# Kernel tuning notes

Hardware: AMD Instinct MI355X
Metric: run time of the kernel (lower is better)

## Reference

```python
import jax, jax.numpy as jnp
from jax import lax
import numpy as np

BATCH, T, IN_DIM, RES = 32, 2048, 64, 1024
SPECTRAL_RADIUS, SPARSITY, INPUT_SCALING, LEAK = 1.2, 0.2, 0.5, 0.3


def setup_inputs() -> dict:
    key = jax.random.key(0)
    inputs = jax.random.normal(key, (BATCH, T, IN_DIM), dtype=jnp.float32)
    # Replicate the layer's build(): fixed random reservoir, seeded numpy RNG.
    rng = np.random.RandomState(42)
    W_in = rng.uniform(-INPUT_SCALING, INPUT_SCALING, size=(IN_DIM, RES)).astype(np.float32)
    W_res = rng.randn(RES, RES)
    mask = rng.rand(RES, RES) < SPARSITY
    W_res *= mask
    sr = np.max(np.abs(np.linalg.eigvals(W_res)))
    if sr > 0:
        W_res *= SPECTRAL_RADIUS / sr
    return {
        "inputs": inputs,
        "W_in": jnp.asarray(W_in),
        "W_res": jnp.asarray(W_res.astype(np.float32)),
    }


def reference(inputs, W_in, W_res):
    # inputs: [B, T, I]; W_in: [I, R]; W_res: [R, R]
    leak = jnp.asarray(LEAK, inputs.dtype)
    # Hoist the input projection out of the recurrence (same math, one big GEMM).
    x_proj = jnp.einsum("bti,ir->btr", inputs, W_in)  # [B, T, R]
    state0 = jnp.zeros((inputs.shape[0], W_res.shape[0]), dtype=inputs.dtype)

    def step(state, x_t):  # x_t: [B, R]
        new_state = jnp.tanh(x_t + state @ W_res)
        state = (1.0 - leak) * state + leak * new_state
        return state, state

    _, states = lax.scan(step, state0, jnp.swapaxes(x_proj, 0, 1))  # [T, B, R]
    return jnp.swapaxes(states, 0, 1)  # [B, T, R] (return_sequences=True)
```

## Files before the change

kernel.cpp:

```cpp
#include <hip/hip_runtime.h>

#define T_STEPS 2048
#define NBATCH  32
#define IN_DIM  64
#define RES     1024
#define LEAKF   0.3f
#define NCG     64
#define NBG     4

typedef unsigned int u32;
typedef unsigned long long u64cp;

__global__ __launch_bounds__(256, 1) void esn_persist(
    const float* __restrict__ inp,
    const float* __restrict__ Win,
    const float* __restrict__ Wres,
    float* __restrict__ out,
    float* __restrict__ sC,
    u32* __restrict__ cnts)
{
    const int tid   = threadIdx.x;
    const int c_loc = tid & 15;
    const int ks    = tid >> 4;
    const int cg    = blockIdx.x;
    const int bg    = blockIdx.y;
    const int c0    = cg * 16;
    const int b0    = bg * 8;
    const int c     = c0 + c_loc;

    float w[64];
    {
        const float* wp = Wres + (size_t)(ks * 64) * RES + c;
        #pragma unroll
        for (int j = 0; j < 64; ++j) w[j] = wp[(size_t)j * RES];
    }

    __shared__ __align__(16) float sst[8256];
    __shared__ float pl[16][8][17];

    u32* cnt = cnts + bg * 64;
    float* sCb = sC + (size_t)bg * 2 * RES * 8;

    const int fb = tid >> 4;
    float s_prev = 0.f;

    for (int t = 0; t < T_STEPS; ++t) {
        float* sCr = sCb + ((t & 1) ^ 1) * (RES * 8);
        float* sCw = sCb + (t & 1) * (RES * 8);

        float x = 0.f;
        if (tid < 128) {
            const float* inb = inp + ((size_t)(b0 + fb) * T_STEPS + t) * IN_DIM;
            #pragma unroll
            for (int i = 0; i < IN_DIM; i += 4) {
                const float4 v = *reinterpret_cast<const float4*>(inb + i);
                x = fmaf(v.x, Win[(size_t)(i + 0) * RES + c], x);
                x = fmaf(v.y, Win[(size_t)(i + 1) * RES + c], x);
                x = fmaf(v.z, Win[(size_t)(i + 2) * RES + c], x);
                x = fmaf(v.w, Win[(size_t)(i + 3) * RES + c], x);
            }
        }

        if (t > 0) {
            if (tid == 0) {
                const u32 tgt = 64u * (u32)t;
                while (__hip_atomic_load(cnt, __ATOMIC_RELAXED,
                                         __HIP_MEMORY_SCOPE_AGENT) < tgt) {
                    __builtin_amdgcn_s_sleep(1);
                }
            }
            __syncthreads();

            #pragma unroll
            for (int i = 0; i < 8; ++i) {
                const int m = i * 256 + tid;
                u64cp lo = __hip_atomic_load((u64cp*)(sCr + (size_t)m * 4),
                                             __ATOMIC_RELAXED, __HIP_MEMORY_SCOPE_AGENT);
                u64cp hi = __hip_atomic_load((u64cp*)(sCr + (size_t)m * 4 + 2),
                                             __ATOMIC_RELAXED, __HIP_MEMORY_SCOPE_AGENT);
                float4* dst = (float4*)((char*)sst + (size_t)m * 16 + (m >> 7) * 16);
                *dst = make_float4(__uint_as_float((unsigned)(lo       )),
                                   __uint_as_float((unsigned)(lo >> 32u)),
                                   __uint_as_float((unsigned)(hi       )),
                                   __uint_as_float((unsigned)(hi >> 32u)));
            }
            __syncthreads();
        }

        float acc0 = 0.f, acc1 = 0.f, acc2 = 0.f, acc3 = 0.f;
        float acc4 = 0.f, acc5 = 0.f, acc6 = 0.f, acc7 = 0.f;
        if (t > 0) {
            const char* base = (const char*)sst + (size_t)(ks * 64) * 32 + ks * 16;
            #pragma unroll
            for (int j = 0; j < 64; ++j) {
                const float4 sa = *reinterpret_cast<const float4*>(base + j * 32);
                const float4 sb = *reinterpret_cast<const float4*>(base + j * 32 + 16);
                const float wj = w[j];
                acc0 = fmaf(sa.x, wj, acc0);
                acc1 = fmaf(sa.y, wj, acc1);
                acc2 = fmaf(sa.z, wj, acc2);
                acc3 = fmaf(sa.w, wj, acc3);
                acc4 = fmaf(sb.x, wj, acc4);
                acc5 = fmaf(sb.y, wj, acc5);
                acc6 = fmaf(sb.z, wj, acc6);
                acc7 = fmaf(sb.w, wj, acc7);
            }
        }

        pl[ks][0][c_loc] = acc0;
        pl[ks][1][c_loc] = acc1;
        pl[ks][2][c_loc] = acc2;
        pl[ks][3][c_loc] = acc3;
        pl[ks][4][c_loc] = acc4;
        pl[ks][5][c_loc] = acc5;
        pl[ks][6][c_loc] = acc6;
        pl[ks][7][c_loc] = acc7;
        __syncthreads();

        if (tid < 128) {
            float sum = 0.f;
            #pragma unroll
            for (int q = 0; q < 16; ++q) sum += pl[q][fb][c_loc];

            const float nw = tanhf(x + sum);
            const float sn = fmaf(1.0f - LEAKF, s_prev, LEAKF * nw);
            s_prev = sn;

            out[((size_t)(b0 + fb) * T_STEPS + t) * RES + c] = sn;
            __hip_atomic_store(sCw + (size_t)c * 8 + fb, sn,
                               __ATOMIC_RELAXED, __HIP_MEMORY_SCOPE_AGENT);
        }
        __syncthreads();

        if (tid == 0)
            __hip_atomic_fetch_add(cnt, 1u, __ATOMIC_RELAXED,
                                   __HIP_MEMORY_SCOPE_AGENT);
    }
}

__global__ __launch_bounds__(256) void esn_step(
    const float* __restrict__ inp,
    const float* __restrict__ Win,
    const float* __restrict__ Wres,
    float* __restrict__ out,
    float* __restrict__ sT,
    int t)
{
    const int tid   = threadIdx.x;
    const int c_loc = tid & 15;
    const int ks    = tid >> 4;
    const int c0    = blockIdx.x * 16;
    const int b0    = blockIdx.y * 8;
    const int c     = c0 + c_loc;

    const float* sTr = sT + ((t & 1) ^ 1) * (RES * NBATCH);
    float*       sTw = sT + (t & 1) * (RES * NBATCH);

    float acc0 = 0.f, acc1 = 0.f, acc2 = 0.f, acc3 = 0.f;
    float acc4 = 0.f, acc5 = 0.f, acc6 = 0.f, acc7 = 0.f;

    if (t > 0) {
        const int kbeg = ks * 64;
        const float* wp = Wres + (size_t)kbeg * RES + c;
        const float* sp = sTr + kbeg * NBATCH + b0;
        #pragma unroll 4
        for (int j = 0; j < 64; ++j) {
            const float w = wp[(size_t)j * RES];
            const float4 sa = *reinterpret_cast<const float4*>(sp + j * NBATCH);
            const float4 sb = *reinterpret_cast<const float4*>(sp + j * NBATCH + 4);
            acc0 = fmaf(sa.x, w, acc0);
            acc1 = fmaf(sa.y, w, acc1);
            acc2 = fmaf(sa.z, w, acc2);
            acc3 = fmaf(sa.w, w, acc3);
            acc4 = fmaf(sb.x, w, acc4);
            acc5 = fmaf(sb.y, w, acc5);
            acc6 = fmaf(sb.z, w, acc6);
            acc7 = fmaf(sb.w, w, acc7);
        }
    }

    __shared__ float plf[16][8][17];
    plf[ks][0][c_loc] = acc0;
    plf[ks][1][c_loc] = acc1;
    plf[ks][2][c_loc] = acc2;
    plf[ks][3][c_loc] = acc3;
    plf[ks][4][c_loc] = acc4;
    plf[ks][5][c_loc] = acc5;
    plf[ks][6][c_loc] = acc6;
    plf[ks][7][c_loc] = acc7;
    __syncthreads();

    if (tid < 128) {
        const int b   = tid >> 4;
        const int cl  = tid & 15;
        const int cgl = c0 + cl;
        const int bgl = b0 + b;

        float sum = 0.f;
        #pragma unroll
        for (int q = 0; q < 16; ++q) sum += plf[q][b][cl];

        const float* inb = inp + ((size_t)bgl * T_STEPS + t) * IN_DIM;
        float x = 0.f;
        #pragma unroll 8
        for (int i = 0; i < IN_DIM; ++i)
            x = fmaf(inb[i], Win[(size_t)i * RES + cgl], x);

        const float nw = tanhf(x + sum);
        const float spv = (t > 0) ? sTr[cgl * NBATCH + bgl] : 0.f;
        const float sn = fmaf(1.0f - LEAKF, spv, LEAKF * nw);

        out[((size_t)bgl * T_STEPS + t) * RES + cgl] = sn;
        sTw[cgl * NBATCH + bgl] = sn;
    }
}

extern "C" void kernel_launch(void* const* d_in, const int* in_sizes, int n_in,
                              void* d_out, int out_size, void* d_ws, size_t ws_size,
                              hipStream_t stream)
{
    const float* inp  = (const float*)d_in[0];
    const float* Win  = (const float*)d_in[1];
    const float* Wres = (const float*)d_in[2];
    float* out = (float*)d_out;

    const size_t cntBytes   = 1024;
    const size_t stateBytes = (size_t)NBG * 2 * RES * 8 * sizeof(float);

    if (ws_size >= cntBytes + stateBytes) {
        u32*   cnts = (u32*)d_ws;
        float* sC   = (float*)((char*)d_ws + cntBytes);
        hipMemsetAsync(cnts, 0, cntBytes, stream);
        hipLaunchKernelGGL(esn_persist, dim3(NCG, NBG), dim3(256), 0, stream,
                           inp, Win, Wres, out, sC, cnts);
        return;
    }

    float* sT = (float*)d_ws;
    dim3 grid(64, 4), blk(256);
    for (int t = 0; t < T_STEPS; ++t) {
        hipLaunchKernelGGL(esn_step, grid, blk, 0, stream,
                           inp, Win, Wres, out, sT, t);
    }
}
```

Baseline: 21.39 ms.

## Use 1024-thread persistent blocks to cut inter-block barrier participants

The persistent kernel now runs 64 blocks of 1024 threads instead of 256 blocks of 256 threads. Each block handles 64 reservoir columns for one batch group, so each group's spin-wait barrier counts 16 arrivals per step instead of 64. The state copy into shared memory becomes unpadded 8-byte atomic loads, relying on wave-wide broadcast reads rather than bank-conflict padding. Each block now does four times more work per step, and register pressure rises under the 1024-thread launch bound.

New measurement: 58.85 ms. +175.2%, slower.

```diff
diff --git a/kernel.cpp b/kernel.cpp
--- a/kernel.cpp
+++ b/kernel.cpp
@@ -5,13 +5,13 @@
 #define IN_DIM  64
 #define RES     1024
 #define LEAKF   0.3f
-#define NCG     64
-#define NBG     4
+#define NGRP    4
+#define BPG     16
 
 typedef unsigned int u32;
 typedef unsigned long long u64cp;
 
-__global__ __launch_bounds__(256, 1) void esn_persist(
+__global__ __launch_bounds__(1024) void esn_persist(
     const float* __restrict__ inp,
     const float* __restrict__ Win,
     const float* __restrict__ Wres,
@@ -20,12 +20,12 @@
     u32* __restrict__ cnts)
 {
     const int tid   = threadIdx.x;
-    const int c_loc = tid & 15;
-    const int ks    = tid >> 4;
-    const int cg    = blockIdx.x;
-    const int bg    = blockIdx.y;
-    const int c0    = cg * 16;
-    const int b0    = bg * 8;
+    const int c_loc = tid & 63;
+    const int ks    = tid >> 6;
+    const int g     = blockIdx.x & 3;
+    const int rank  = blockIdx.x >> 2;
+    const int c0    = rank * 64;
+    const int b0    = g * 8;
     const int c     = c0 + c_loc;
 
     float w[64];
@@ -35,13 +35,13 @@
         for (int j = 0; j < 64; ++j) w[j] = wp[(size_t)j * RES];
     }
 
-    __shared__ __align__(16) float sst[8256];
-    __shared__ float pl[16][8][17];
-
-    u32* cnt = cnts + bg * 64;
-    float* sCb = sC + (size_t)bg * 2 * RES * 8;
-
-    const int fb = tid >> 4;
+    __shared__ __align__(16) float sst[RES * 8];
+    __shared__ float pl[16][8][64];
+
+    u32* cnt = cnts + g * 64;
+    float* sCb = sC + (size_t)g * 2 * RES * 8;
+
+    const int fb = ks;
     float s_prev = 0.f;
 
     for (int t = 0; t < T_STEPS; ++t) {
@@ -49,7 +49,7 @@
         float* sCw = sCb + (t & 1) * (RES * 8);
 
         float x = 0.f;
-        if (tid < 128) {
+        if (tid < 512) {
             const float* inb = inp + ((size_t)(b0 + fb) * T_STEPS + t) * IN_DIM;
             #pragma unroll
             for (int i = 0; i < IN_DIM; i += 4) {
@@ -63,7 +63,7 @@
 
         if (t > 0) {
             if (tid == 0) {
-                const u32 tgt = 64u * (u32)t;
+                const u32 tgt = (u32)BPG * (u32)t;
                 while (__hip_atomic_load(cnt, __ATOMIC_RELAXED,
                                          __HIP_MEMORY_SCOPE_AGENT) < tgt) {
                     __builtin_amdgcn_s_sleep(1);
@@ -72,17 +72,11 @@
             __syncthreads();
 
             #pragma unroll
-            for (int i = 0; i < 8; ++i) {
-                const int m = i * 256 + tid;
-                u64cp lo = __hip_atomic_load((u64cp*)(sCr + (size_t)m * 4),
-                                             __ATOMIC_RELAXED, __HIP_MEMORY_SCOPE_AGENT);
-                u64cp hi = __hip_atomic_load((u64cp*)(sCr + (size_t)m * 4 + 2),
-                                             __ATOMIC_RELAXED, __HIP_MEMORY_SCOPE_AGENT);
-                float4* dst = (float4*)((char*)sst + (size_t)m * 16 + (m >> 7) * 16);
-                *dst = make_float4(__uint_as_float((unsigned)(lo       )),
-                                   __uint_as_float((unsigned)(lo >> 32u)),
-                                   __uint_as_float((unsigned)(hi       )),
-                                   __uint_as_float((unsigned)(hi >> 32u)));
+            for (int q = 0; q < 4; ++q) {
+                const int mw = q * 1024 + tid;
+                const u64cp v = __hip_atomic_load((const u64cp*)sCr + mw,
+                                    __ATOMIC_RELAXED, __HIP_MEMORY_SCOPE_AGENT);
+                reinterpret_cast<u64cp*>(sst)[mw] = v;
             }
             __syncthreads();
         }
@@ -90,11 +84,11 @@
         float acc0 = 0.f, acc1 = 0.f, acc2 = 0.f, acc3 = 0.f;
         float acc4 = 0.f, acc5 = 0.f, acc6 = 0.f, acc7 = 0.f;
         if (t > 0) {
-            const char* base = (const char*)sst + (size_t)(ks * 64) * 32 + ks * 16;
+            const float* base = sst + ks * 512;
             #pragma unroll
             for (int j = 0; j < 64; ++j) {
-                const float4 sa = *reinterpret_cast<const float4*>(base + j * 32);
-                const float4 sb = *reinterpret_cast<const float4*>(base + j * 32 + 16);
+                const float4 sa = *reinterpret_cast<const float4*>(base + j * 8);
+                const float4 sb = *reinterpret_cast<const float4*>(base + j * 8 + 4);
                 const float wj = w[j];
                 acc0 = fmaf(sa.x, wj, acc0);
                 acc1 = fmaf(sa.y, wj, acc1);
@@ -117,7 +111,7 @@
         pl[ks][7][c_loc] = acc7;
         __syncthreads();
 
-        if (tid < 128) {
+        if (tid < 512) {
             float sum = 0.f;
             #pragma unroll
             for (int q = 0; q < 16; ++q) sum += pl[q][fb][c_loc];
@@ -225,13 +219,13 @@
     float* out = (float*)d_out;
 
     const size_t cntBytes   = 1024;
-    const size_t stateBytes = (size_t)NBG * 2 * RES * 8 * sizeof(float);
+    const size_t stateBytes = (size_t)NGRP * 2 * RES * 8 * sizeof(float);
 
     if (ws_size >= cntBytes + stateBytes) {
         u32*   cnts = (u32*)d_ws;
         float* sC   = (float*)((char*)d_ws + cntBytes);
         hipMemsetAsync(cnts, 0, cntBytes, stream);
-        hipLaunchKernelGGL(esn_persist, dim3(NCG, NBG), dim3(256), 0, stream,
+        hipLaunchKernelGGL(esn_persist, dim3(NGRP * BPG), dim3(1024), 0, stream,
                            inp, Win, Wres, out, sC, cnts);
         return;
     }
```
